# Kernel optimization log

Measured on AMD Instinct MI355X. Metric: run time of the kernel, lower is better.

## Reference

```python
import jax, jax.numpy as jnp
import numpy as np

D_MODEL = 1024
H = 16
D_K = D_MODEL // H
WINDOW = 256
NEG = -1e9


def setup_inputs() -> dict:
    key = jax.random.key(0)
    ks = jax.random.split(key, 7)
    B, S = 2, 4096
    sc = 0.02
    return {
        "q": jax.random.normal(ks[0], (B, S, D_MODEL), jnp.float32),
        "k": jax.random.normal(ks[1], (B, S, D_MODEL), jnp.float32),
        "v": jax.random.normal(ks[2], (B, S, D_MODEL), jnp.float32),
        "wq": jax.random.normal(ks[3], (D_MODEL, D_MODEL), jnp.float32) * sc,
        "wk": jax.random.normal(ks[4], (D_MODEL, D_MODEL), jnp.float32) * sc,
        "wv": jax.random.normal(ks[5], (D_MODEL, D_MODEL), jnp.float32) * sc,
        "wo": jax.random.normal(ks[6], (D_MODEL, D_MODEL), jnp.float32) * sc,
    }


def _local_mask(seq_len: int, window_size: int):
    left = (window_size - 1) // 2
    right = window_size - 1 - left
    idx = jnp.arange(seq_len)
    dist = jnp.abs(idx[None, :] - idx[:, None])
    return (dist <= left) | (dist <= right)  # [S, S] bool


def reference(q, k, v, wq, wk, wv, wo):
    B, S, _ = q.shape
    # torch Linear: x @ W.T
    def proj(x, w):
        return (x @ w.T).reshape(B, S, H, D_K).transpose(0, 2, 1, 3)  # [B,H,S,Dk]
    Q, K, V = proj(q, wq), proj(k, wk), proj(v, wv)
    scores = jnp.einsum("bhqd,bhkd->bhqk", Q, K) / jnp.sqrt(jnp.float32(D_K))
    mask = _local_mask(S, WINDOW)
    scores = jnp.where(mask[None, None], scores, NEG)
    attn = jax.nn.softmax(scores, axis=-1)
    x = jnp.einsum("bhqk,bhkd->bhqd", attn, V)
    x = x.transpose(0, 2, 1, 3).reshape(B, S, D_MODEL)
    return x @ wo.T
```

## Files before the change

### kernel.cpp

```cpp
#include <hip/hip_runtime.h>
#include <hip/hip_bf16.h>

#define S_LEN 4096
#define B_SZ 2
#define DM 1024
#define NH 16
#define DH 64

typedef __attribute__((ext_vector_type(8))) short short8;
typedef __attribute__((ext_vector_type(4))) float f32x4;

__device__ __forceinline__ ushort f2b(float f) {
  union { __hip_bfloat16 b; ushort u; } cv;
  cv.b = __float2bfloat16(f);
  return cv.u;
}

__device__ __forceinline__ void glds16(const ushort* g, ushort* l) {
  __builtin_amdgcn_global_load_lds(
      (const __attribute__((address_space(1))) void*)g,
      (__attribute__((address_space(3))) void*)l, 16, 0, 0);
}

__global__ void cvt_all(const float* __restrict__ q, const float* __restrict__ k,
                        const float* __restrict__ v, const float* __restrict__ wq,
                        const float* __restrict__ wk, const float* __restrict__ wv,
                        const float* __restrict__ wo, ushort* __restrict__ dst) {
  const int NX4 = 2097152;
  const int NW4 = 262144;
  const int total = 3 * NX4 + 4 * NW4;
  for (int i = blockIdx.x * blockDim.x + threadIdx.x; i < total;
       i += gridDim.x * blockDim.x) {
    const float* s;
    int j;
    if (i < NX4) { s = q; j = i; }
    else if (i < 2 * NX4) { s = k; j = i - NX4; }
    else if (i < 3 * NX4) { s = v; j = i - 2 * NX4; }
    else {
      int t = i - 3 * NX4;
      int wsel = t >> 18;
      j = t & (NW4 - 1);
      s = wsel == 0 ? wq : wsel == 1 ? wk : wsel == 2 ? wv : wo;
    }
    float4 val = reinterpret_cast<const float4*>(s)[j];
    ushort4 o;
    o.x = f2b(val.x); o.y = f2b(val.y); o.z = f2b(val.z); o.w = f2b(val.w);
    reinterpret_cast<ushort4*>(dst)[i] = o;
  }
}

__device__ __forceinline__ short8 ldsrd(const ushort* base, int row, int cb) {
  const int pcb = cb ^ ((row & 7) << 4);
  return *reinterpret_cast<const short8*>(
      reinterpret_cast<const char*>(base) + row * 128 + pcb);
}

template <int MODE>
__launch_bounds__(512, 2)
__global__ void gemmP(const ushort* __restrict__ A0, const ushort* __restrict__ A1,
                      const ushort* __restrict__ A2, const ushort* __restrict__ W0,
                      const ushort* __restrict__ W1, const ushort* __restrict__ W2,
                      void* __restrict__ O0, void* __restrict__ O1,
                      void* __restrict__ O2) {
  __shared__ ushort As[3][16384];
  __shared__ ushort Bs[3][8192];
  const int tid = threadIdx.x;
  const int lane = tid & 63, w = tid >> 6;
  const int wm = w >> 1, wn = w & 1;
  const int g = lane >> 4, lr = lane & 15;
  const int m0 = blockIdx.x * 256;
  const int ysel = (MODE == 0) ? (blockIdx.y >> 3) : 0;
  const ushort* A = (MODE == 0) ? (ysel == 0 ? A0 : ysel == 1 ? A1 : A2) : A0;
  const ushort* W = (MODE == 0) ? (ysel == 0 ? W0 : ysel == 1 ? W1 : W2) : W0;
  const int n0 = ((MODE == 0) ? (blockIdx.y & 7) : blockIdx.y) * 128;

  const int row_r = tid >> 3;
  const int cb = ((tid & 7) * 16) ^ ((row_r & 7) << 4);
  const ushort* Asrc = A + (size_t)(m0 + row_r) * DM + (cb >> 1);
  const ushort* Wsrc = W + (size_t)(n0 + row_r) * DM + (cb >> 1);

#define STG_ALL(bs, kt)                                                      \
  { const int kq = (kt) * 64;                                                \
    glds16(Asrc + kq,                        &As[bs][w * 512]);              \
    glds16(Asrc + (size_t)64 * DM + kq,      &As[bs][4096 + w * 512]);       \
    glds16(Asrc + (size_t)128 * DM + kq,     &As[bs][8192 + w * 512]);       \
    glds16(Asrc + (size_t)192 * DM + kq,     &As[bs][12288 + w * 512]);      \
    glds16(Wsrc + kq,                        &Bs[bs][w * 512]);              \
    glds16(Wsrc + (size_t)64 * DM + kq,      &Bs[bs][4096 + w * 512]); }

  f32x4 acc[4][4] = {};
  short8 af[4][2], b0[2][2], b1[2][2];

  STG_ALL(0, 0);
  STG_ALL(1, 1);

  int bc = 0;
  for (int kt = 0; kt < 16; ++kt) {
    const int bs = bc >= 1 ? bc - 1 : bc + 2;
    const int tn = kt + 2 < 16 ? kt + 2 : 15;
    asm volatile("s_waitcnt vmcnt(6)" ::: "memory");
    __builtin_amdgcn_s_barrier();
    __builtin_amdgcn_sched_barrier(0);
    const ushort* Ab = &As[bc][0];
    const ushort* Bb = &Bs[bc][0];
#pragma unroll
    for (int m = 0; m < 4; m++)
#pragma unroll
      for (int kk = 0; kk < 2; kk++)
        af[m][kk] = ldsrd(Ab, wm * 64 + m * 16 + lr, kk * 64 + g * 16);
#pragma unroll
    for (int n = 0; n < 2; n++)
#pragma unroll
      for (int kk = 0; kk < 2; kk++) {
        b0[n][kk] = ldsrd(Bb, wn * 64 + n * 16 + lr, kk * 64 + g * 16);
        b1[n][kk] = ldsrd(Bb, wn * 64 + 32 + n * 16 + lr, kk * 64 + g * 16);
      }
    STG_ALL(bs, tn);
    __builtin_amdgcn_sched_barrier(0);
    asm volatile("s_waitcnt lgkmcnt(0)" ::: "memory");
    __builtin_amdgcn_sched_barrier(0);
    __builtin_amdgcn_s_setprio(1);
#pragma unroll
    for (int m = 0; m < 4; m++)
#pragma unroll
      for (int n = 0; n < 2; n++)
#pragma unroll
        for (int kk = 0; kk < 2; kk++)
          acc[m][n] = __builtin_amdgcn_mfma_f32_16x16x32_bf16(af[m][kk], b0[n][kk],
                                                              acc[m][n], 0, 0, 0);
#pragma unroll
    for (int m = 0; m < 4; m++)
#pragma unroll
      for (int n = 0; n < 2; n++)
#pragma unroll
        for (int kk = 0; kk < 2; kk++)
          acc[m][2 + n] = __builtin_amdgcn_mfma_f32_16x16x32_bf16(af[m][kk], b1[n][kk],
                                                                  acc[m][2 + n], 0, 0, 0);
    __builtin_amdgcn_s_setprio(0);
    __builtin_amdgcn_sched_barrier(0);
    bc = bc + 1 == 3 ? 0 : bc + 1;
  }
#undef STG_ALL

  const int colB = n0 + wn * 64;
#pragma unroll
  for (int m = 0; m < 4; ++m) {
    const int row0 = m0 + wm * 64 + m * 16 + g * 4;
#pragma unroll
    for (int n = 0; n < 4; ++n) {
      const int col = colB + n * 16 + lr;
      if (MODE == 2) {
#pragma unroll
        for (int r = 0; r < 4; r++)
          reinterpret_cast<float*>(O0)[(size_t)(row0 + r) * DM + col] = acc[m][n][r];
      } else if (ysel == 0 || ysel == 1) {
        ushort* O = reinterpret_cast<ushort*>(ysel == 0 ? O0 : O1);
#pragma unroll
        for (int r = 0; r < 4; r++)
          O[(size_t)(row0 + r) * DM + col] = f2b(acc[m][n][r]);
      } else {
        const int b = row0 >> 12, s0 = row0 & 4095;
        const int h = col >> 6, dk = col & 63;
        ushort4 o;
        o.x = f2b(acc[m][n][0]); o.y = f2b(acc[m][n][1]);
        o.z = f2b(acc[m][n][2]); o.w = f2b(acc[m][n][3]);
        *reinterpret_cast<ushort4*>(
            reinterpret_cast<ushort*>(O2) +
            (((size_t)(b * NH + h) * DH + dk) << 12) + s0) = o;
      }
    }
  }
}

__global__ void attn_local(const ushort* __restrict__ Qp, const ushort* __restrict__ Kp,
                           const ushort* __restrict__ Vt, ushort* __restrict__ Ao) {
  __shared__ ushort Ks[2][4096];
  __shared__ ushort Vs[2][4096];
  __shared__ ushort Ps[8][16 * 72];
  const int tid = threadIdx.x;
  const int lane = tid & 63;
  const int w = tid >> 6;
  const int g = lane >> 4, lr = lane & 15;
  const int bh = blockIdx.y, b = bh >> 4, h = bh & 15;
  const int qt = ((blockIdx.x & 7) << 2) + (blockIdx.x >> 3);
  const int q0 = qt * 128;

  const float C_SCALE = 0.125f * 1.44269504f;
  const float C_M = 8.0f * 1.44269504f;

  const int qrow = q0 + w * 16 + lr;
  const ushort* qptr = Qp + ((size_t)b * S_LEN + qrow) * DM + h * DH;
  short8 qf[2];
  qf[0] = *reinterpret_cast<const short8*>(qptr + g * 8);
  qf[1] = *reinterpret_cast<const short8*>(qptr + 32 + g * 8);

  float l_r[4] = {0.f, 0.f, 0.f, 0.f};
  f32x4 acc_o[4] = {};

  const int sr = tid >> 3;
  const int scb = (tid & 7) * 16;

  const int t_lo = q0 >= 128 ? q0 - 128 : 0;
  const int t_hi = (q0 + 256) <= S_LEN ? (q0 + 256) : S_LEN;

#define STAGE(bb, kk0)                                                        \
  {                                                                           \
    const int cbk = scb ^ ((sr & 7) << 4);                                    \
    glds16(Kp + ((size_t)b * S_LEN + (kk0) + sr) * DM + h * DH + cbk / 2,     \
           &Ks[bb][w * 512]);                                                 \
    glds16(Vt + (((size_t)bh * DH + sr) << 12) + (kk0) + cbk / 2,             \
           &Vs[bb][w * 512]);                                                 \
  }

  STAGE(0, t_lo);

  int it = 0;
  for (int k0 = t_lo; k0 < t_hi; k0 += 64, ++it) {
    const int cur = it & 1;
    asm volatile("s_waitcnt vmcnt(0)" ::: "memory");
    __builtin_amdgcn_s_barrier();
    __builtin_amdgcn_sched_barrier(0);
    if (k0 + 64 < t_hi) STAGE(cur ^ 1, k0 + 64);
    __builtin_amdgcn_sched_barrier(0);

    f32x4 sc[4] = {};
    __builtin_amdgcn_s_setprio(1);
#pragma unroll
    for (int kk = 0; kk < 2; kk++) {
#pragma unroll
      for (int nt = 0; nt < 4; nt++) {
        const int kr = nt * 16 + lr;
        const int cbk = (kk * 64 + g * 16) ^ ((kr & 7) << 4);
        short8 kf = *reinterpret_cast<const short8*>(
            reinterpret_cast<const char*>(&Ks[cur][0]) + kr * 128 + cbk);
        sc[nt] = __builtin_amdgcn_mfma_f32_16x16x32_bf16(qf[kk], kf, sc[nt], 0, 0, 0);
      }
    }
    __builtin_amdgcn_s_setprio(0);
    const bool edge = (k0 < q0) || (k0 > q0 + 64);
    if (edge) {
#pragma unroll
      for (int nt = 0; nt < 4; nt++) {
        const int key = k0 + nt * 16 + lr;
#pragma unroll
        for (int r = 0; r < 4; r++) {
          const int qr = q0 + w * 16 + g * 4 + r;
          int d = qr - key; d = d < 0 ? -d : d;
          float arg = fmaf(sc[nt][r], C_SCALE, -C_M);
          arg = (d <= 128) ? arg : -400.f;
          const float p = exp2f(arg);
          sc[nt][r] = p;
          l_r[r] += p;
        }
      }
    } else {
#pragma unroll
      for (int nt = 0; nt < 4; nt++)
#pragma unroll
        for (int r = 0; r < 4; r++) {
          const float p = exp2f(fmaf(sc[nt][r], C_SCALE, -C_M));
          sc[nt][r] = p;
          l_r[r] += p;
        }
    }

    ushort* myP = Ps[w];
#pragma unroll
    for (int nt = 0; nt < 4; nt++)
#pragma unroll
      for (int r = 0; r < 4; r++)
        myP[(g * 4 + r) * 72 + nt * 16 + lr] = f2b(sc[nt][r]);
    asm volatile("s_waitcnt lgkmcnt(0)" ::: "memory");
    __builtin_amdgcn_sched_barrier(0);

    __builtin_amdgcn_s_setprio(1);
#pragma unroll
    for (int kk = 0; kk < 2; kk++) {
      short8 pf2 = *reinterpret_cast<const short8*>(myP + lr * 72 + kk * 32 + g * 8);
#pragma unroll
      for (int nt = 0; nt < 4; nt++) {
        const int vr = nt * 16 + lr;
        const int cbk = (kk * 64 + g * 16) ^ ((vr & 7) << 4);
        short8 vf = *reinterpret_cast<const short8*>(
            reinterpret_cast<const char*>(&Vs[cur][0]) + vr * 128 + cbk);
        acc_o[nt] = __builtin_amdgcn_mfma_f32_16x16x32_bf16(pf2, vf, acc_o[nt], 0, 0, 0);
      }
    }
    __builtin_amdgcn_s_setprio(0);
  }
#undef STAGE

  float inv[4];
#pragma unroll
  for (int r = 0; r < 4; r++) {
    float l = l_r[r];
    l += __shfl_xor(l, 1);
    l += __shfl_xor(l, 2);
    l += __shfl_xor(l, 4);
    l += __shfl_xor(l, 8);
    inv[r] = 1.0f / l;
  }
  const int qr0 = q0 + w * 16 + g * 4;
  ushort* orow = Ao + (size_t)b * S_LEN * DM + h * DH;
#pragma unroll
  for (int nt = 0; nt < 4; nt++)
#pragma unroll
    for (int r = 0; r < 4; r++)
      orow[(size_t)(qr0 + r) * DM + nt * 16 + lr] = f2b(acc_o[nt][r] * inv[r]);
}

extern "C" void kernel_launch(void* const* d_in, const int* in_sizes, int n_in,
                              void* d_out, int out_size, void* d_ws, size_t ws_size,
                              hipStream_t stream) {
  const float* q  = (const float*)d_in[0];
  const float* k  = (const float*)d_in[1];
  const float* v  = (const float*)d_in[2];
  const float* wq = (const float*)d_in[3];
  const float* wk = (const float*)d_in[4];
  const float* wv = (const float*)d_in[5];
  const float* wo = (const float*)d_in[6];

  const size_t NX = (size_t)B_SZ * S_LEN * DM;
  const size_t NW = (size_t)DM * DM;
  if (ws_size < (7 * NX + 4 * NW) * sizeof(ushort)) return;

  ushort* ws  = (ushort*)d_ws;
  ushort* qb  = ws;
  ushort* kb  = qb + NX;
  ushort* vb  = kb + NX;
  ushort* wqb = vb + NX;
  ushort* wkb = wqb + NW;
  ushort* wvb = wkb + NW;
  ushort* wob = wvb + NW;
  ushort* Qp  = wob + NW;
  ushort* Kp  = Qp + NX;
  ushort* Vt  = Kp + NX;
  ushort* Ao  = Vt + NX;

  cvt_all<<<dim3(2048), dim3(256), 0, stream>>>(q, k, v, wq, wk, wv, wo, ws);

  gemmP<0><<<dim3(32, 24), dim3(512), 0, stream>>>(qb, kb, vb, wqb, wkb, wvb,
                                                   Qp, Kp, Vt);

  attn_local<<<dim3(32, 32), dim3(512), 0, stream>>>(Qp, Kp, Vt, Ao);

  gemmP<2><<<dim3(32, 8), dim3(512), 0, stream>>>(Ao, Ao, Ao, wob, wob, wob,
                                                  d_out, d_out, d_out);
}
```

Before: 150.3 us.

## Use 256x256 tiles with quadrant-phased pipeline for QKV projection GEMM

The fused QKV projection GEMM moves from 256x128 tiles with a triple-buffered stage to 256x256 tiles. Each block uses a double-buffered LDS split into halves, and each k-step runs four MFMA phases, one per quadrant, each interleaved with partial global-to-LDS loads and barriers. Larger tiles raise arithmetic intensity and halve the grid, at the cost of more accumulator registers, more barriers, and fewer blocks (384) to fill the CUs. The output projection keeps the old design as a separate non-templated kernel.

Result: slower. 163.5 us (+8.8%).

```diff
diff --git a/kernel.cpp b/kernel.cpp
--- a/kernel.cpp
+++ b/kernel.cpp
@@ -55,106 +55,163 @@
       reinterpret_cast<const char*>(base) + row * 128 + pcb);
 }
 
-template <int MODE>
 __launch_bounds__(512, 2)
-__global__ void gemmP(const ushort* __restrict__ A0, const ushort* __restrict__ A1,
+__global__ void gemmF(const ushort* __restrict__ A0, const ushort* __restrict__ A1,
                       const ushort* __restrict__ A2, const ushort* __restrict__ W0,
                       const ushort* __restrict__ W1, const ushort* __restrict__ W2,
-                      void* __restrict__ O0, void* __restrict__ O1,
-                      void* __restrict__ O2) {
-  __shared__ ushort As[3][16384];
-  __shared__ ushort Bs[3][8192];
+                      ushort* __restrict__ O0, ushort* __restrict__ O1,
+                      ushort* __restrict__ O2) {
+  __shared__ ushort As[2][2][8192];
+  __shared__ ushort Bs[2][2][8192];
   const int tid = threadIdx.x;
   const int lane = tid & 63, w = tid >> 6;
-  const int wm = w >> 1, wn = w & 1;
+  const int wm = w >> 2, wn = w & 3;
   const int g = lane >> 4, lr = lane & 15;
   const int m0 = blockIdx.x * 256;
-  const int ysel = (MODE == 0) ? (blockIdx.y >> 3) : 0;
-  const ushort* A = (MODE == 0) ? (ysel == 0 ? A0 : ysel == 1 ? A1 : A2) : A0;
-  const ushort* W = (MODE == 0) ? (ysel == 0 ? W0 : ysel == 1 ? W1 : W2) : W0;
-  const int n0 = ((MODE == 0) ? (blockIdx.y & 7) : blockIdx.y) * 128;
-
-  const int row_r = tid >> 3;
-  const int cb = ((tid & 7) * 16) ^ ((row_r & 7) << 4);
-  const ushort* Asrc = A + (size_t)(m0 + row_r) * DM + (cb >> 1);
-  const ushort* Wsrc = W + (size_t)(n0 + row_r) * DM + (cb >> 1);
-
-#define STG_ALL(bs, kt)                                                      \
-  { const int kq = (kt) * 64;                                                \
-    glds16(Asrc + kq,                        &As[bs][w * 512]);              \
-    glds16(Asrc + (size_t)64 * DM + kq,      &As[bs][4096 + w * 512]);       \
-    glds16(Asrc + (size_t)128 * DM + kq,     &As[bs][8192 + w * 512]);       \
-    glds16(Asrc + (size_t)192 * DM + kq,     &As[bs][12288 + w * 512]);      \
-    glds16(Wsrc + kq,                        &Bs[bs][w * 512]);              \
-    glds16(Wsrc + (size_t)64 * DM + kq,      &Bs[bs][4096 + w * 512]); }
-
-  f32x4 acc[4][4] = {};
+  const int ysel = blockIdx.y >> 2;
+  const ushort* A = ysel == 0 ? A0 : ysel == 1 ? A1 : A2;
+  const ushort* W = ysel == 0 ? W0 : ysel == 1 ? W1 : W2;
+  const int n0 = (blockIdx.y & 3) * 256;
+
+  const int r0 = tid >> 3;
+  const int cbs = ((tid & 7) * 16) ^ ((r0 & 7) << 4);
+  const ushort* Asrc = A + (size_t)(m0 + r0) * DM + (cbs >> 1);
+  const ushort* Wsrc = W + (size_t)(n0 + r0) * DM + (cbs >> 1);
+
+#define STG_A(nb, h, ktv)                                                     \
+  { const int kq = (ktv) * 64;                                                \
+    glds16(Asrc + (size_t)((h) * 128) * DM + kq, &As[nb][h][w * 512]);        \
+    glds16(Asrc + (size_t)((h) * 128 + 64) * DM + kq,                         \
+           &As[nb][h][4096 + w * 512]); }
+#define STG_B(nb, h, ktv)                                                     \
+  { const int kq = (ktv) * 64;                                                \
+    glds16(Wsrc + (size_t)((h) * 128) * DM + kq, &Bs[nb][h][w * 512]);        \
+    glds16(Wsrc + (size_t)((h) * 128 + 64) * DM + kq,                         \
+           &Bs[nb][h][4096 + w * 512]); }
+
+  f32x4 acc[8][4] = {};
   short8 af[4][2], b0[2][2], b1[2][2];
 
-  STG_ALL(0, 0);
-  STG_ALL(1, 1);
-
-  int bc = 0;
+  STG_B(0, 0, 0); STG_B(0, 1, 0);
+  STG_A(0, 0, 0); STG_A(0, 1, 0);
+  STG_B(1, 0, 1); STG_B(1, 1, 1);
+  asm volatile("s_waitcnt vmcnt(4)" ::: "memory");
+  __builtin_amdgcn_s_barrier();
+  __builtin_amdgcn_sched_barrier(0);
+
   for (int kt = 0; kt < 16; ++kt) {
-    const int bs = bc >= 1 ? bc - 1 : bc + 2;
-    const int tn = kt + 2 < 16 ? kt + 2 : 15;
-    asm volatile("s_waitcnt vmcnt(6)" ::: "memory");
-    __builtin_amdgcn_s_barrier();
-    __builtin_amdgcn_sched_barrier(0);
-    const ushort* Ab = &As[bc][0];
-    const ushort* Bb = &Bs[bc][0];
-#pragma unroll
-    for (int m = 0; m < 4; m++)
+    const int cur = kt & 1;
+    const int nxa = (kt + 1) & 1;
+    const int ta = kt + 1 < 16 ? kt + 1 : 15;
+    const int tb = kt + 2 < 16 ? kt + 2 : 15;
+    const ushort* Abh = &As[cur][wm][0];
+    const ushort* Bbh = &Bs[cur][wn >> 1][0];
+    const int brow = (wn & 1) * 64;
+
+#pragma unroll
+    for (int mf = 0; mf < 4; mf++)
 #pragma unroll
       for (int kk = 0; kk < 2; kk++)
-        af[m][kk] = ldsrd(Ab, wm * 64 + m * 16 + lr, kk * 64 + g * 16);
-#pragma unroll
-    for (int n = 0; n < 2; n++)
-#pragma unroll
-      for (int kk = 0; kk < 2; kk++) {
-        b0[n][kk] = ldsrd(Bb, wn * 64 + n * 16 + lr, kk * 64 + g * 16);
-        b1[n][kk] = ldsrd(Bb, wn * 64 + 32 + n * 16 + lr, kk * 64 + g * 16);
-      }
-    STG_ALL(bs, tn);
-    __builtin_amdgcn_sched_barrier(0);
+        af[mf][kk] = ldsrd(Abh, mf * 16 + lr, kk * 64 + g * 16);
+#pragma unroll
+    for (int nf = 0; nf < 2; nf++)
+#pragma unroll
+      for (int kk = 0; kk < 2; kk++)
+        b0[nf][kk] = ldsrd(Bbh, brow + nf * 16 + lr, kk * 64 + g * 16);
+    STG_A(nxa, 0, ta);
+    __builtin_amdgcn_sched_barrier(0);
+    __builtin_amdgcn_s_barrier();
     asm volatile("s_waitcnt lgkmcnt(0)" ::: "memory");
     __builtin_amdgcn_sched_barrier(0);
     __builtin_amdgcn_s_setprio(1);
 #pragma unroll
-    for (int m = 0; m < 4; m++)
-#pragma unroll
-      for (int n = 0; n < 2; n++)
-#pragma unroll
-        for (int kk = 0; kk < 2; kk++)
-          acc[m][n] = __builtin_amdgcn_mfma_f32_16x16x32_bf16(af[m][kk], b0[n][kk],
-                                                              acc[m][n], 0, 0, 0);
-#pragma unroll
-    for (int m = 0; m < 4; m++)
-#pragma unroll
-      for (int n = 0; n < 2; n++)
-#pragma unroll
-        for (int kk = 0; kk < 2; kk++)
-          acc[m][2 + n] = __builtin_amdgcn_mfma_f32_16x16x32_bf16(af[m][kk], b1[n][kk],
-                                                                  acc[m][2 + n], 0, 0, 0);
-    __builtin_amdgcn_s_setprio(0);
-    __builtin_amdgcn_sched_barrier(0);
-    bc = bc + 1 == 3 ? 0 : bc + 1;
-  }
-#undef STG_ALL
+    for (int mf = 0; mf < 4; mf++)
+#pragma unroll
+      for (int nf = 0; nf < 2; nf++)
+#pragma unroll
+        for (int kk = 0; kk < 2; kk++)
+          acc[mf][nf] = __builtin_amdgcn_mfma_f32_16x16x32_bf16(
+              af[mf][kk], b0[nf][kk], acc[mf][nf], 0, 0, 0);
+    __builtin_amdgcn_s_setprio(0);
+    __builtin_amdgcn_sched_barrier(0);
+    __builtin_amdgcn_s_barrier();
+
+#pragma unroll
+    for (int nf = 0; nf < 2; nf++)
+#pragma unroll
+      for (int kk = 0; kk < 2; kk++)
+        b1[nf][kk] = ldsrd(Bbh, brow + 32 + nf * 16 + lr, kk * 64 + g * 16);
+    STG_A(nxa, 1, ta);
+    __builtin_amdgcn_sched_barrier(0);
+    __builtin_amdgcn_s_barrier();
+    asm volatile("s_waitcnt lgkmcnt(0)" ::: "memory");
+    __builtin_amdgcn_sched_barrier(0);
+    __builtin_amdgcn_s_setprio(1);
+#pragma unroll
+    for (int mf = 0; mf < 4; mf++)
+#pragma unroll
+      for (int nf = 0; nf < 2; nf++)
+#pragma unroll
+        for (int kk = 0; kk < 2; kk++)
+          acc[mf][2 + nf] = __builtin_amdgcn_mfma_f32_16x16x32_bf16(
+              af[mf][kk], b1[nf][kk], acc[mf][2 + nf], 0, 0, 0);
+    __builtin_amdgcn_s_setprio(0);
+    __builtin_amdgcn_sched_barrier(0);
+    __builtin_amdgcn_s_barrier();
+
+#pragma unroll
+    for (int mf = 0; mf < 4; mf++)
+#pragma unroll
+      for (int kk = 0; kk < 2; kk++)
+        af[mf][kk] = ldsrd(Abh, 64 + mf * 16 + lr, kk * 64 + g * 16);
+    STG_B(cur, 0, tb);
+    __builtin_amdgcn_sched_barrier(0);
+    __builtin_amdgcn_s_barrier();
+    asm volatile("s_waitcnt lgkmcnt(0)" ::: "memory");
+    __builtin_amdgcn_sched_barrier(0);
+    __builtin_amdgcn_s_setprio(1);
+#pragma unroll
+    for (int mf = 0; mf < 4; mf++)
+#pragma unroll
+      for (int nf = 0; nf < 2; nf++)
+#pragma unroll
+        for (int kk = 0; kk < 2; kk++)
+          acc[4 + mf][2 + nf] = __builtin_amdgcn_mfma_f32_16x16x32_bf16(
+              af[mf][kk], b1[nf][kk], acc[4 + mf][2 + nf], 0, 0, 0);
+    __builtin_amdgcn_s_setprio(0);
+    __builtin_amdgcn_sched_barrier(0);
+    __builtin_amdgcn_s_barrier();
+
+    STG_B(cur, 1, tb);
+    asm volatile("s_waitcnt vmcnt(4)" ::: "memory");
+    __builtin_amdgcn_sched_barrier(0);
+    __builtin_amdgcn_s_barrier();
+    __builtin_amdgcn_sched_barrier(0);
+    __builtin_amdgcn_s_setprio(1);
+#pragma unroll
+    for (int mf = 0; mf < 4; mf++)
+#pragma unroll
+      for (int nf = 0; nf < 2; nf++)
+#pragma unroll
+        for (int kk = 0; kk < 2; kk++)
+          acc[4 + mf][nf] = __builtin_amdgcn_mfma_f32_16x16x32_bf16(
+              af[mf][kk], b0[nf][kk], acc[4 + mf][nf], 0, 0, 0);
+    __builtin_amdgcn_s_setprio(0);
+    __builtin_amdgcn_sched_barrier(0);
+    __builtin_amdgcn_s_barrier();
+  }
+#undef STG_A
+#undef STG_B
 
   const int colB = n0 + wn * 64;
 #pragma unroll
-  for (int m = 0; m < 4; ++m) {
-    const int row0 = m0 + wm * 64 + m * 16 + g * 4;
+  for (int m = 0; m < 8; ++m) {
+    const int row0 = m0 + wm * 128 + m * 16 + g * 4;
 #pragma unroll
     for (int n = 0; n < 4; ++n) {
       const int col = colB + n * 16 + lr;
-      if (MODE == 2) {
-#pragma unroll
-        for (int r = 0; r < 4; r++)
-          reinterpret_cast<float*>(O0)[(size_t)(row0 + r) * DM + col] = acc[m][n][r];
-      } else if (ysel == 0 || ysel == 1) {
-        ushort* O = reinterpret_cast<ushort*>(ysel == 0 ? O0 : O1);
+      if (ysel == 0 || ysel == 1) {
+        ushort* O = ysel == 0 ? O0 : O1;
 #pragma unroll
         for (int r = 0; r < 4; r++)
           O[(size_t)(row0 + r) * DM + col] = f2b(acc[m][n][r]);
@@ -165,9 +222,102 @@
         o.x = f2b(acc[m][n][0]); o.y = f2b(acc[m][n][1]);
         o.z = f2b(acc[m][n][2]); o.w = f2b(acc[m][n][3]);
         *reinterpret_cast<ushort4*>(
-            reinterpret_cast<ushort*>(O2) +
-            (((size_t)(b * NH + h) * DH + dk) << 12) + s0) = o;
+            O2 + (((size_t)(b * NH + h) * DH + dk) << 12) + s0) = o;
       }
+    }
+  }
+}
+
+__launch_bounds__(512, 2)
+__global__ void gemmP2(const ushort* __restrict__ A, const ushort* __restrict__ W,
+                       float* __restrict__ Of) {
+  __shared__ ushort As[3][16384];
+  __shared__ ushort Bs[3][8192];
+  const int tid = threadIdx.x;
+  const int lane = tid & 63, w = tid >> 6;
+  const int wm = w >> 1, wn = w & 1;
+  const int g = lane >> 4, lr = lane & 15;
+  const int m0 = blockIdx.x * 256;
+  const int n0 = blockIdx.y * 128;
+
+  const int row_r = tid >> 3;
+  const int cb = ((tid & 7) * 16) ^ ((row_r & 7) << 4);
+  const ushort* Asrc = A + (size_t)(m0 + row_r) * DM + (cb >> 1);
+  const ushort* Wsrc = W + (size_t)(n0 + row_r) * DM + (cb >> 1);
+
+#define STG_ALL(bs, kt)                                                      \
+  { const int kq = (kt) * 64;                                                \
+    glds16(Asrc + kq,                        &As[bs][w * 512]);              \
+    glds16(Asrc + (size_t)64 * DM + kq,      &As[bs][4096 + w * 512]);       \
+    glds16(Asrc + (size_t)128 * DM + kq,     &As[bs][8192 + w * 512]);       \
+    glds16(Asrc + (size_t)192 * DM + kq,     &As[bs][12288 + w * 512]);      \
+    glds16(Wsrc + kq,                        &Bs[bs][w * 512]);              \
+    glds16(Wsrc + (size_t)64 * DM + kq,      &Bs[bs][4096 + w * 512]); }
+
+  f32x4 acc[4][4] = {};
+  short8 af[4][2], b0[2][2], b1[2][2];
+
+  STG_ALL(0, 0);
+  STG_ALL(1, 1);
+
+  int bc = 0;
+  for (int kt = 0; kt < 16; ++kt) {
+    const int bs = bc >= 1 ? bc - 1 : bc + 2;
+    const int tn = kt + 2 < 16 ? kt + 2 : 15;
+    asm volatile("s_waitcnt vmcnt(6)" ::: "memory");
+    __builtin_amdgcn_s_barrier();
+    __builtin_amdgcn_sched_barrier(0);
+    const ushort* Ab = &As[bc][0];
+    const ushort* Bb = &Bs[bc][0];
+#pragma unroll
+    for (int m = 0; m < 4; m++)
+#pragma unroll
+      for (int kk = 0; kk < 2; kk++)
+        af[m][kk] = ldsrd(Ab, wm * 64 + m * 16 + lr, kk * 64 + g * 16);
+#pragma unroll
+    for (int n = 0; n < 2; n++)
+#pragma unroll
+      for (int kk = 0; kk < 2; kk++) {
+        b0[n][kk] = ldsrd(Bb, wn * 64 + n * 16 + lr, kk * 64 + g * 16);
+        b1[n][kk] = ldsrd(Bb, wn * 64 + 32 + n * 16 + lr, kk * 64 + g * 16);
+      }
+    STG_ALL(bs, tn);
+    __builtin_amdgcn_sched_barrier(0);
+    asm volatile("s_waitcnt lgkmcnt(0)" ::: "memory");
+    __builtin_amdgcn_sched_barrier(0);
+    __builtin_amdgcn_s_setprio(1);
+#pragma unroll
+    for (int m = 0; m < 4; m++)
+#pragma unroll
+      for (int n = 0; n < 2; n++)
+#pragma unroll
+        for (int kk = 0; kk < 2; kk++)
+          acc[m][n] = __builtin_amdgcn_mfma_f32_16x16x32_bf16(af[m][kk], b0[n][kk],
+                                                              acc[m][n], 0, 0, 0);
+#pragma unroll
+    for (int m = 0; m < 4; m++)
+#pragma unroll
+      for (int n = 0; n < 2; n++)
+#pragma unroll
+        for (int kk = 0; kk < 2; kk++)
+          acc[m][2 + n] = __builtin_amdgcn_mfma_f32_16x16x32_bf16(af[m][kk], b1[n][kk],
+                                                                  acc[m][2 + n], 0, 0, 0);
+    __builtin_amdgcn_s_setprio(0);
+    __builtin_amdgcn_sched_barrier(0);
+    bc = bc + 1 == 3 ? 0 : bc + 1;
+  }
+#undef STG_ALL
+
+  const int colB = n0 + wn * 64;
+#pragma unroll
+  for (int m = 0; m < 4; ++m) {
+    const int row0 = m0 + wm * 64 + m * 16 + g * 4;
+#pragma unroll
+    for (int n = 0; n < 4; ++n) {
+      const int col = colB + n * 16 + lr;
+#pragma unroll
+      for (int r = 0; r < 4; r++)
+        Of[(size_t)(row0 + r) * DM + col] = acc[m][n][r];
     }
   }
 }
@@ -339,11 +489,10 @@
 
   cvt_all<<<dim3(2048), dim3(256), 0, stream>>>(q, k, v, wq, wk, wv, wo, ws);
 
-  gemmP<0><<<dim3(32, 24), dim3(512), 0, stream>>>(qb, kb, vb, wqb, wkb, wvb,
-                                                   Qp, Kp, Vt);
+  gemmF<<<dim3(32, 12), dim3(512), 0, stream>>>(qb, kb, vb, wqb, wkb, wvb,
+                                                Qp, Kp, Vt);
 
   attn_local<<<dim3(32, 32), dim3(512), 0, stream>>>(Qp, Kp, Vt, Ao);
 
-  gemmP<2><<<dim3(32, 8), dim3(512), 0, stream>>>(Ao, Ao, Ao, wob, wob, wob,
-                                                  d_out, d_out, d_out);
-}
+  gemmP2<<<dim3(32, 8), dim3(512), 0, stream>>>(Ao, wob, (float*)d_out);
+}
```

## Widen attention key tile to 128 and stage V inside the iteration

Applied to the files above, without the earlier changes.

The local-attention kernel now processes 128 keys per iteration instead of 64, which halves the number of loop iterations and top-of-loop barriers. K stays double-buffered with a 128-row prefetch. V becomes a single buffer laid out as 256-byte rows: it is loaded at the start of each iteration and overlaps with the QK MFMAs and softmax, guarded by a partial vmcnt wait and an extra barrier. The P·V product is split into two 64-key halves through the per-wave P scratch. The trade-off is V load latency exposed within each iteration and more registers for the doubled score tile, which may hurt occupancy.

Result: no change. 152.3 us (+1.3%).

```diff
diff --git a/kernel.cpp b/kernel.cpp
--- a/kernel.cpp
+++ b/kernel.cpp
@@ -174,8 +174,8 @@
 
 __global__ void attn_local(const ushort* __restrict__ Qp, const ushort* __restrict__ Kp,
                            const ushort* __restrict__ Vt, ushort* __restrict__ Ao) {
-  __shared__ ushort Ks[2][4096];
-  __shared__ ushort Vs[2][4096];
+  __shared__ ushort Ks[2][8192];
+  __shared__ ushort Vs[8192];
   __shared__ ushort Ps[8][16 * 72];
   const int tid = threadIdx.x;
   const int lane = tid & 63;
@@ -199,48 +199,56 @@
 
   const int sr = tid >> 3;
   const int scb = (tid & 7) * 16;
+  const int cbk = scb ^ ((sr & 7) << 4);
+  const int vrow = tid >> 4;
+  const int vcb = ((tid & 15) * 16) ^ ((vrow & 7) << 4);
 
   const int t_lo = q0 >= 128 ? q0 - 128 : 0;
   const int t_hi = (q0 + 256) <= S_LEN ? (q0 + 256) : S_LEN;
 
-#define STAGE(bb, kk0)                                                        \
-  {                                                                           \
-    const int cbk = scb ^ ((sr & 7) << 4);                                    \
-    glds16(Kp + ((size_t)b * S_LEN + (kk0) + sr) * DM + h * DH + cbk / 2,     \
+#define STAGE_K(bb, kk0)                                                      \
+  { glds16(Kp + ((size_t)b * S_LEN + (kk0) + sr) * DM + h * DH + cbk / 2,     \
            &Ks[bb][w * 512]);                                                 \
-    glds16(Vt + (((size_t)bh * DH + sr) << 12) + (kk0) + cbk / 2,             \
-           &Vs[bb][w * 512]);                                                 \
-  }
-
-  STAGE(0, t_lo);
+    glds16(Kp + ((size_t)b * S_LEN + (kk0) + 64 + sr) * DM + h * DH + cbk / 2,\
+           &Ks[bb][4096 + w * 512]); }
+#define STAGE_V(kk0)                                                          \
+  { glds16(Vt + (((size_t)bh * DH + vrow) << 12) + (kk0) + vcb / 2,           \
+           &Vs[w * 512]);                                                     \
+    glds16(Vt + (((size_t)bh * DH + 32 + vrow) << 12) + (kk0) + vcb / 2,      \
+           &Vs[4096 + w * 512]); }
+
+  STAGE_K(0, t_lo);
 
   int it = 0;
-  for (int k0 = t_lo; k0 < t_hi; k0 += 64, ++it) {
+  for (int k0 = t_lo; k0 < t_hi; k0 += 128, ++it) {
     const int cur = it & 1;
+    const bool pfK = (k0 + 128 < t_hi);
     asm volatile("s_waitcnt vmcnt(0)" ::: "memory");
     __builtin_amdgcn_s_barrier();
     __builtin_amdgcn_sched_barrier(0);
-    if (k0 + 64 < t_hi) STAGE(cur ^ 1, k0 + 64);
-    __builtin_amdgcn_sched_barrier(0);
-
-    f32x4 sc[4] = {};
+    if (pfK) STAGE_K(cur ^ 1, k0 + 128);
+    STAGE_V(k0);
+    __builtin_amdgcn_sched_barrier(0);
+
+    f32x4 sc[8] = {};
     __builtin_amdgcn_s_setprio(1);
 #pragma unroll
     for (int kk = 0; kk < 2; kk++) {
 #pragma unroll
-      for (int nt = 0; nt < 4; nt++) {
+      for (int nt = 0; nt < 8; nt++) {
         const int kr = nt * 16 + lr;
-        const int cbk = (kk * 64 + g * 16) ^ ((kr & 7) << 4);
+        const int cb2 = (kk * 64 + g * 16) ^ ((kr & 7) << 4);
         short8 kf = *reinterpret_cast<const short8*>(
-            reinterpret_cast<const char*>(&Ks[cur][0]) + kr * 128 + cbk);
+            reinterpret_cast<const char*>(&Ks[cur][0]) + kr * 128 + cb2);
         sc[nt] = __builtin_amdgcn_mfma_f32_16x16x32_bf16(qf[kk], kf, sc[nt], 0, 0, 0);
       }
     }
     __builtin_amdgcn_s_setprio(0);
-    const bool edge = (k0 < q0) || (k0 > q0 + 64);
+
+    const bool edge = (k0 != q0);
     if (edge) {
 #pragma unroll
-      for (int nt = 0; nt < 4; nt++) {
+      for (int nt = 0; nt < 8; nt++) {
         const int key = k0 + nt * 16 + lr;
 #pragma unroll
         for (int r = 0; r < 4; r++) {
@@ -255,7 +263,7 @@
       }
     } else {
 #pragma unroll
-      for (int nt = 0; nt < 4; nt++)
+      for (int nt = 0; nt < 8; nt++)
 #pragma unroll
         for (int r = 0; r < 4; r++) {
           const float p = exp2f(fmaf(sc[nt][r], C_SCALE, -C_M));
@@ -264,31 +272,43 @@
         }
     }
 
+    if (pfK) {
+      asm volatile("s_waitcnt vmcnt(2)" ::: "memory");
+    } else {
+      asm volatile("s_waitcnt vmcnt(0)" ::: "memory");
+    }
+    __builtin_amdgcn_s_barrier();
+    __builtin_amdgcn_sched_barrier(0);
+
     ushort* myP = Ps[w];
 #pragma unroll
-    for (int nt = 0; nt < 4; nt++)
-#pragma unroll
-      for (int r = 0; r < 4; r++)
-        myP[(g * 4 + r) * 72 + nt * 16 + lr] = f2b(sc[nt][r]);
-    asm volatile("s_waitcnt lgkmcnt(0)" ::: "memory");
-    __builtin_amdgcn_sched_barrier(0);
-
-    __builtin_amdgcn_s_setprio(1);
-#pragma unroll
-    for (int kk = 0; kk < 2; kk++) {
-      short8 pf2 = *reinterpret_cast<const short8*>(myP + lr * 72 + kk * 32 + g * 8);
-#pragma unroll
-      for (int nt = 0; nt < 4; nt++) {
-        const int vr = nt * 16 + lr;
-        const int cbk = (kk * 64 + g * 16) ^ ((vr & 7) << 4);
-        short8 vf = *reinterpret_cast<const short8*>(
-            reinterpret_cast<const char*>(&Vs[cur][0]) + vr * 128 + cbk);
-        acc_o[nt] = __builtin_amdgcn_mfma_f32_16x16x32_bf16(pf2, vf, acc_o[nt], 0, 0, 0);
-      }
-    }
-    __builtin_amdgcn_s_setprio(0);
-  }
-#undef STAGE
+    for (int hh = 0; hh < 2; ++hh) {
+#pragma unroll
+      for (int nt = 0; nt < 4; nt++)
+#pragma unroll
+        for (int r = 0; r < 4; r++)
+          myP[(g * 4 + r) * 72 + nt * 16 + lr] = f2b(sc[hh * 4 + nt][r]);
+      asm volatile("s_waitcnt lgkmcnt(0)" ::: "memory");
+      __builtin_amdgcn_sched_barrier(0);
+      __builtin_amdgcn_s_setprio(1);
+#pragma unroll
+      for (int kk2 = 0; kk2 < 2; kk2++) {
+        short8 pf2 = *reinterpret_cast<const short8*>(myP + lr * 72 + kk2 * 32 + g * 8);
+#pragma unroll
+        for (int nt = 0; nt < 4; nt++) {
+          const int vr = nt * 16 + lr;
+          const int pcb = (hh * 128 + kk2 * 64 + g * 16) ^ ((vr & 7) << 4);
+          short8 vf = *reinterpret_cast<const short8*>(
+              reinterpret_cast<const char*>(&Vs[0]) + vr * 256 + pcb);
+          acc_o[nt] = __builtin_amdgcn_mfma_f32_16x16x32_bf16(pf2, vf, acc_o[nt], 0, 0, 0);
+        }
+      }
+      __builtin_amdgcn_s_setprio(0);
+      __builtin_amdgcn_sched_barrier(0);
+    }
+  }
+#undef STAGE_K
+#undef STAGE_V
 
   float inv[4];
 #pragma unroll
```
